# Kernel optimization log

Hardware: AMD Instinct MI355X
Metric: run time of the kernel (lower is better)

## Reference

```python
import jax, jax.numpy as jnp
import numpy as np

N, E, D, H = 15000, 300000, 128, 4
Dh = D // H
EPS = 1e-5

def gelu(x):
    return jax.nn.gelu(x, approximate=False)

def lin(x, W, b=None):
    y = x @ W.T
    return y + b if b is not None else y

def bnorm(x, g, b):
    # BatchNorm1d (training stats, biased var) over the row dim
    m = x.mean(0)
    v = x.var(0)
    return (x - m) * jax.lax.rsqrt(v + EPS) * g + b

def setup_inputs() -> dict:
    key = jax.random.key(0)
    ks = iter(jax.random.split(key, 64))
    def W(o, i):
        return jax.random.normal(next(ks), (o, i), jnp.float32) / jnp.sqrt(i)
    z = lambda o: jnp.zeros((o,), jnp.float32)
    o1 = lambda o: jnp.ones((o,), jnp.float32)
    inp = {
        'h_V': jax.random.normal(next(ks), (N, D), jnp.float32),
        'h_E': jax.random.normal(next(ks), (E, D), jnp.float32),
        'edge_idx': jax.random.randint(next(ks), (2, E), 0, N, jnp.int64),
        'batch_id': jnp.sort(jax.random.randint(next(ks), (N,), 0, 30, jnp.int32)),
        # NeighborAttention.W_V MLP: num_in(256)->128->128->128
        'Wv1': W(D, 2 * D), 'bv1': z(D), 'Wv2': W(D, D), 'bv2': z(D), 'Wv3': W(D, D), 'bv3': z(D),
        # NeighborAttention.Bias MLP: 3*128->128->128->num_heads
        'Wb1': W(D, 3 * D), 'bb1': z(D), 'Wb2': W(D, D), 'bb2': z(D), 'Wb3': W(H, D), 'bb3': z(H),
        # W_O (no bias)
        'Wo': W(D, D),
        # norms 0/1 on nodes
        'g0': o1(D), 'b0': z(D), 'g1': o1(D), 'b1': z(D),
        # dense FFN 128->512->128
        'Wd1': W(4 * D, D), 'bd1': z(4 * D), 'Wd2': W(D, 4 * D), 'bd2': z(D),
        # EdgeMLP: 384->128->128->128 plus edge norm
        'We1': W(D, 3 * D), 'be1': z(D), 'We2': W(D, D), 'be2': z(D), 'We3': W(D, D), 'be3': z(D),
        'ge': o1(D), 'bEn': z(D),
    }
    return inp

def reference(h_V, h_E, edge_idx, batch_id,
              Wv1, bv1, Wv2, bv2, Wv3, bv3,
              Wb1, bb1, Wb2, bb2, Wb3, bb3,
              Wo, g0, b0, g1, b1,
              Wd1, bd1, Wd2, bd2,
              We1, be1, We2, be2, We3, be3, ge, bEn):
    src, dst = edge_idx[0], edge_idx[1]
    # --- NeighborAttention (sparse) ---
    h_EV = jnp.concatenate([h_E, h_V[dst]], axis=-1)              # (E, 2D)
    bias_in = jnp.concatenate([h_V[src], h_EV], axis=-1)          # (E, 3D)
    w = lin(gelu(lin(gelu(lin(bias_in, Wb1, bb1)), Wb2, bb2)), Wb3, bb3)
    w = w * (1.0 / jnp.sqrt(jnp.float32(Dh)))                     # (E, H)
    V = lin(gelu(lin(gelu(lin(h_EV, Wv1, bv1)), Wv2, bv2)), Wv3, bv3).reshape(E, H, Dh)
    # scatter_softmax over edges grouped by src (center_id)
    m = jax.ops.segment_max(w, src, num_segments=N)               # (N, H)
    e = jnp.exp(w - m[src])
    s = jax.ops.segment_sum(e, src, num_segments=N)
    attend = e / s[src]                                           # (E, H)
    agg = jax.ops.segment_sum(attend[..., None] * V, src, num_segments=N).reshape(N, D)
    dh = agg @ Wo.T
    # --- residual + norm + FFN ---
    h_V = bnorm(h_V + dh, g0, b0)
    dh = lin(gelu(lin(h_V, Wd1, bd1)), Wd2, bd2)
    h_V = bnorm(h_V + dh, g1, b1)
    # --- EdgeMLP update ---
    h_EV2 = jnp.concatenate([h_V[src], h_E, h_V[dst]], axis=-1)   # (E, 3D)
    msg = lin(gelu(lin(gelu(lin(h_EV2, We1, be1)), We2, be2)), We3, be3)
    h_E = bnorm(h_E + msg, ge, bEn)
    # Context with node_context=edge_context=0 is a no-op
    return h_V, h_E
```

## Files before the change

### kernel.cpp

```cpp
#include <hip/hip_runtime.h>
#include <hip/hip_bf16.h>
#include <math.h>


#define NN 15000
#define EE 300000

typedef short s16x8 __attribute__((ext_vector_type(8)));
typedef float f32x4 __attribute__((ext_vector_type(4)));
#define MFMA16(a,b,c) __builtin_amdgcn_mfma_f32_16x16x32_bf16((a),(b),(c),0,0,0)

#define O_Wot  0
#define O_Wd1t (O_Wot  + 128*128)
#define O_Wd2t (O_Wd1t + 128*512)
#define O_BF   (O_Wd2t + 512*128)
#define O_WB   (O_BF + 107520)
#define O_M    (O_WB + EE*4)
#define O_S    (O_M + NN*4)
#define O_AGG  (O_S + NN*4)
#define O_STAT (O_AGG + NN*128)
#define O_AB   (O_STAT + 768)
#define O_XB   (O_AB + 768)
#define O_HID  (O_XB + NN*128)
#define O_PERM (O_HID + NN*512)
#define O_CNT  (O_PERM + EE)
#define O_CUR  (O_CNT + 15360)

#define UB_Wb1 0
#define UB_Wb2 49152
#define UB_Wb3 65536
#define UB_Wv1 67584
#define UB_Wv2 100352
#define UB_Wv3 116736
#define UB_We1 133120
#define UB_We2 182272
#define UB_We3 198656

__device__ inline float gelu_f(float x){
  return 0.5f*x*(1.0f + erff(x*0.70710678118654752f));
}
__device__ inline unsigned fenc(float f){
  unsigned u = __float_as_uint(f);
  return (u & 0x80000000u) ? ~u : (u | 0x80000000u);
}
__device__ inline float fdec(unsigned u){
  return __uint_as_float((u & 0x80000000u) ? (u & 0x7fffffffu) : ~u);
}
__device__ inline ushort bfb(float f){
  __bf16 h = (__bf16)f;
  return __builtin_bit_cast(unsigned short, h);
}


struct EMem {
  ushort act[128][128];
  int   idx[256];
  float cp[256];
};

struct EMemC {
  union { ushort act[128][128]; float vbuf[128][128]; };
  int pe[128];
  int idx[256];
};

union FB { s16x8 v; ushort u[8]; };

__device__ inline s16x8 load_x8(const float* __restrict__ p){
  float4 a = *(const float4*)p;
  float4 b = *(const float4*)(p+4);
  FB r;
  r.u[0]=bfb(a.x); r.u[1]=bfb(a.y); r.u[2]=bfb(a.z); r.u[3]=bfb(a.w);
  r.u[4]=bfb(b.x); r.u[5]=bfb(b.y); r.u[6]=bfb(b.z); r.u[7]=bfb(b.w);
  return r.v;
}

__device__ inline void st_act4(ushort (*act)[128], int e, int obase,
                               float g0,float g1,float g2,float g3){
  short4 s;
  s.x=(short)bfb(g0); s.y=(short)bfb(g1); s.z=(short)bfb(g2); s.w=(short)bfb(g3);
  *(short4*)&act[e][obase ^ ((e&7)<<3)] = s;
}
__device__ inline s16x8 ld_act(ushort (*act)[128], int e, int k0){
  return *(const s16x8*)&act[e][k0 ^ ((e&7)<<3)];
}

__device__ inline void zacc(f32x4 (&a)[4][4]){
  #pragma unroll
  for(int i=0;i<4;++i)
    #pragma unroll
    for(int j=0;j<4;++j) a[i][j] = (f32x4){0.f,0.f,0.f,0.f};
}

__device__ inline void mm_lds(const ushort* __restrict__ Wb, ushort (*act)[128],
                              int wm, int wn, int el, int kq, f32x4 (&acc)[4][4])
{
  #pragma unroll
  for (int kt=0; kt<4; ++kt){
    s16x8 af[4], bfr[4];
    #pragma unroll
    for (int mt=0;mt<4;++mt)
      af[mt] = *(const s16x8*)&Wb[(wm*64+mt*16+el)*128 + kt*32 + kq*8];
    #pragma unroll
    for (int nt=0;nt<4;++nt)
      bfr[nt] = ld_act(act, wn*64+nt*16+el, kt*32+kq*8);
    #pragma unroll
    for (int mt=0;mt<4;++mt)
      #pragma unroll
      for (int nt=0;nt<4;++nt)
        acc[mt][nt] = MFMA16(af[mt], bfr[nt], acc[mt][nt]);
  }
}

__device__ inline void intf(f32x4 (&acc)[4][4], const float* __restrict__ bias,
                            ushort (*act)[128], int wm, int wn, int el, int kq)
{
  #pragma unroll
  for (int mt=0;mt<4;++mt){
    int obase = wm*64+mt*16+kq*4;
    float4 bb = *(const float4*)&bias[obase];
    #pragma unroll
    for (int nt=0;nt<4;++nt){
      int e = wn*64+nt*16+el;
      st_act4(act, e, obase,
        gelu_f(acc[mt][nt][0]+bb.x), gelu_f(acc[mt][nt][1]+bb.y),
        gelu_f(acc[mt][nt][2]+bb.z), gelu_f(acc[mt][nt][3]+bb.w));
    }
  }
}

__device__ inline void edge_l1_3seg(const float* __restrict__ gV, const float* __restrict__ gI,
    const int* idx, const ushort* __restrict__ W1, int rowbase,
    int wm, int wn, int el, int kq, f32x4 (&acc)[4][4])
{
  #pragma unroll
  for (int seg=0; seg<3; ++seg){
    const float* rp[4];
    #pragma unroll
    for (int nt=0; nt<4; ++nt){
      int eloc = wn*64+nt*16+el;
      int g;
      if (seg==0) g = idx[eloc];
      else if (seg==1){ int e=rowbase+eloc; g = (e<EE)?e:(EE-1); }
      else g = idx[128+eloc];
      rp[nt] = ((seg==1)?gI:gV) + (size_t)g*128 + kq*8;
    }
    #pragma unroll
    for (int kt=0; kt<4; ++kt){
      s16x8 af[4], bfr[4];
      #pragma unroll
      for (int mt=0;mt<4;++mt)
        af[mt] = *(const s16x8*)&W1[(wm*64+mt*16+el)*384 + seg*128 + kt*32 + kq*8];
      #pragma unroll
      for (int nt=0;nt<4;++nt)
        bfr[nt] = load_x8(rp[nt] + kt*32);
      #pragma unroll
      for (int mt=0;mt<4;++mt)
        #pragma unroll
        for (int nt=0;nt<4;++nt)
          acc[mt][nt] = MFMA16(af[mt], bfr[nt], acc[mt][nt]);
    }
  }
}

__global__ void kHist(const int* __restrict__ eidx, int* __restrict__ cnt){
  int e = blockIdx.x*256 + threadIdx.x;
  if (e < EE) atomicAdd(&cnt[eidx[e]], 1);
}

__global__ void kScan(const int* __restrict__ cnt, int* __restrict__ cur){
  __shared__ int part[256];
  __shared__ int excl[256];
  int t = threadIdx.x;
  int base = t*60;
  int s = 0;
  for (int i=0;i<60;++i) s += cnt[base+i];
  part[t] = s;
  __syncthreads();
  if (t==0){ int r=0; for (int i=0;i<256;++i){ excl[i]=r; r+=part[i]; } }
  __syncthreads();
  int run = excl[t];
  for (int i=0;i<60;++i){ int c = cnt[base+i]; cur[base+i] = run; run += c; }
}

__global__ void kScat(const int* __restrict__ eidx, int* __restrict__ cur,
                      int* __restrict__ perm){
  int e = blockIdx.x*256 + threadIdx.x;
  if (e < EE){
    int p = atomicAdd(&cur[eidx[e]], 1);
    perm[p] = e;
  }
}

__global__ void kA_mfma(const float* __restrict__ hV, const float* __restrict__ hE,
    const int* __restrict__ eidx,
    const ushort* __restrict__ W1, const ushort* __restrict__ W2, const ushort* __restrict__ W3,
    const float* __restrict__ b1, const float* __restrict__ b2, const float* __restrict__ b3,
    float* __restrict__ wbuf, unsigned* __restrict__ mArr)
{
  __shared__ EMem sm;
  int t = threadIdx.x, lane = t&63, wave = t>>6;
  int el = lane&15, kq = lane>>4, wm = wave>>1, wn = wave&1;
  int rowbase = blockIdx.x*128;
  if (t<128){ int e=rowbase+t; if(e>=EE) e=EE-1; sm.idx[t]=eidx[e]; sm.idx[128+t]=eidx[EE+e]; }
  __syncthreads();
  f32x4 acc[4][4]; zacc(acc);
  edge_l1_3seg(hV, hE, sm.idx, W1, rowbase, wm, wn, el, kq, acc);
  intf(acc, b1, sm.act, wm, wn, el, kq);
  __syncthreads();
  zacc(acc);
  mm_lds(W2, sm.act, wm, wn, el, kq, acc);
  __syncthreads();
  intf(acc, b2, sm.act, wm, wn, el, kq);
  __syncthreads();
  f32x4 a3[2]; a3[0]=(f32x4){0.f,0.f,0.f,0.f}; a3[1]=(f32x4){0.f,0.f,0.f,0.f};
  #pragma unroll
  for (int kt=0;kt<4;++kt){
    s16x8 af = *(const s16x8*)&W3[el*128 + kt*32 + kq*8];
    #pragma unroll
    for (int q=0;q<2;++q){
      s16x8 bv = ld_act(sm.act, wave*32+q*16+el, kt*32+kq*8);
      a3[q] = MFMA16(af, bv, a3[q]);
    }
  }
  if (kq==0){
    #pragma unroll
    for (int q=0;q<2;++q){
      int eloc = wave*32+q*16+el, e = rowbase+eloc;
      if (e<EE){
        const float SC = 0.17677669529663687f;
        float4 w;
        w.x=(a3[q][0]+b3[0])*SC; w.y=(a3[q][1]+b3[1])*SC;
        w.z=(a3[q][2]+b3[2])*SC; w.w=(a3[q][3]+b3[3])*SC;
        *(float4*)&wbuf[e*4] = w;
        unsigned s4 = (unsigned)sm.idx[eloc]*4;
        atomicMax(&mArr[s4+0],fenc(w.x));
        atomicMax(&mArr[s4+1],fenc(w.y));
        atomicMax(&mArr[s4+2],fenc(w.z));
        atomicMax(&mArr[s4+3],fenc(w.w));
      }
    }
  }
}

__global__ void kB(const int* __restrict__ eidx, const unsigned* __restrict__ mArr,
                   float* __restrict__ wbuf, float* __restrict__ sArr)
{
  int tid = blockIdx.x*256 + threadIdx.x;
  if (tid >= EE*4) return;
  int e = tid >> 2, h = tid & 3;
  int srcn = eidx[e];
  float ex = expf(wbuf[tid] - fdec(mArr[srcn*4 + h]));
  wbuf[tid] = ex;
  atomicAdd(&sArr[srcn*4 + h], ex);
}

__global__ void kC_mfma(const float* __restrict__ hV, const float* __restrict__ hE,
    const int* __restrict__ eidx, const int* __restrict__ perm,
    const ushort* __restrict__ W1, const ushort* __restrict__ W2, const ushort* __restrict__ W3,
    const float* __restrict__ b1, const float* __restrict__ b2, const float* __restrict__ b3,
    const float* __restrict__ wbuf, const float* __restrict__ sArr,
    float* __restrict__ agg)
{
  __shared__ EMemC sm;
  int t = threadIdx.x, lane = t&63, wave = t>>6;
  int el = lane&15, kq = lane>>4, wm = wave>>1, wn = wave&1;
  int rowbase = blockIdx.x*128;
  if (t<128){
    int slot = rowbase + t; if (slot >= EE) slot = EE-1;
    int pe = perm[slot];
    sm.pe[t] = pe;
    sm.idx[t] = eidx[pe];
    sm.idx[128+t] = eidx[EE+pe];
  }
  __syncthreads();
  f32x4 acc[4][4]; zacc(acc);
  #pragma unroll
  for (int seg=0; seg<2; ++seg){
    const float* rp[4];
    #pragma unroll
    for (int nt=0; nt<4; ++nt){
      int eloc = wn*64+nt*16+el;
      int g = (seg==0) ? sm.pe[eloc] : sm.idx[128+eloc];
      rp[nt] = ((seg==0)?hE:hV) + (size_t)g*128 + kq*8;
    }
    #pragma unroll
    for (int kt=0; kt<4; ++kt){
      s16x8 af[4], bfr[4];
      #pragma unroll
      for (int mt=0;mt<4;++mt)
        af[mt] = *(const s16x8*)&W1[(wm*64+mt*16+el)*256 + seg*128 + kt*32 + kq*8];
      #pragma unroll
      for (int nt=0;nt<4;++nt)
        bfr[nt] = load_x8(rp[nt] + kt*32);
      #pragma unroll
      for (int mt=0;mt<4;++mt)
        #pragma unroll
        for (int nt=0;nt<4;++nt)
          acc[mt][nt] = MFMA16(af[mt], bfr[nt], acc[mt][nt]);
    }
  }
  intf(acc, b1, sm.act, wm, wn, el, kq);
  __syncthreads();
  zacc(acc);
  mm_lds(W2, sm.act, wm, wn, el, kq, acc);
  __syncthreads();
  intf(acc, b2, sm.act, wm, wn, el, kq);
  __syncthreads();
  zacc(acc);
  mm_lds(W3, sm.act, wm, wn, el, kq, acc);
  __syncthreads();
  #pragma unroll
  for (int nt=0;nt<4;++nt){
    int e = wn*64+nt*16+el;
    int slot = rowbase + e;
    float at4[4];
    if (slot < EE){
      int pe = sm.pe[e];
      int sn = sm.idx[e];
      float4 wv = *(const float4*)&wbuf[pe*4];
      float4 sv = *(const float4*)&sArr[sn*4];
      at4[0]=wv.x/sv.x; at4[1]=wv.y/sv.y; at4[2]=wv.z/sv.z; at4[3]=wv.w/sv.w;
    } else {
      at4[0]=at4[1]=at4[2]=at4[3]=0.f;
    }
    #pragma unroll
    for (int mt=0;mt<4;++mt){
      int o = wm*64+mt*16+kq*4;
      float4 bb = *(const float4*)&b3[o];
      float a = at4[o>>5];
      float4 v;
      v.x = a*(acc[mt][nt][0]+bb.x);
      v.y = a*(acc[mt][nt][1]+bb.y);
      v.z = a*(acc[mt][nt][2]+bb.z);
      v.w = a*(acc[mt][nt][3]+bb.w);
      *(float4*)&sm.vbuf[e][o ^ ((e&7)<<2)] = v;
    }
  }
  __syncthreads();
  {
    int col = t & 127, h2 = t >> 7;
    int e0 = h2*64;
    float run = 0.f;
    int cursrc = sm.idx[e0];
    for (int e = e0; e < e0+64; ++e){
      int s = sm.idx[e];
      if (s != cursrc){
        atomicAdd(&agg[(size_t)cursrc*128 + col], run);
        run = 0.f; cursrc = s;
      }
      run += sm.vbuf[e][col ^ ((e&7)<<2)];
    }
    atomicAdd(&agg[(size_t)cursrc*128 + col], run);
  }
}

__global__ void kI_mfma(const float* __restrict__ hVfin, const float* __restrict__ hE,
    const int* __restrict__ eidx,
    const ushort* __restrict__ W1, const ushort* __restrict__ W2, const ushort* __restrict__ W3,
    const float* __restrict__ b1, const float* __restrict__ b2, const float* __restrict__ b3,
    float* __restrict__ hEout, float* __restrict__ stat)
{
  __shared__ EMem sm;
  int t = threadIdx.x, lane = t&63, wave = t>>6;
  int el = lane&15, kq = lane>>4, wm = wave>>1, wn = wave&1;
  int rowbase = blockIdx.x*128;
  if (t<128){ int e=rowbase+t; if(e>=EE) e=EE-1; sm.idx[t]=eidx[e]; sm.idx[128+t]=eidx[EE+e]; }
  __syncthreads();
  f32x4 acc[4][4]; zacc(acc);
  edge_l1_3seg(hVfin, hE, sm.idx, W1, rowbase, wm, wn, el, kq, acc);
  intf(acc, b1, sm.act, wm, wn, el, kq);
  __syncthreads();
  zacc(acc);
  mm_lds(W2, sm.act, wm, wn, el, kq, acc);
  __syncthreads();
  intf(acc, b2, sm.act, wm, wn, el, kq);
  __syncthreads();
  zacc(acc);
  mm_lds(W3, sm.act, wm, wn, el, kq, acc);
  float ps[4][4], pq[4][4];
  #pragma unroll
  for (int mt=0;mt<4;++mt)
    #pragma unroll
    for (int r=0;r<4;++r){ ps[mt][r]=0.f; pq[mt][r]=0.f; }
  #pragma unroll
  for (int nt=0;nt<4;++nt){
    int eloc = wn*64+nt*16+el, e = rowbase+eloc;
    if (e < EE){
      #pragma unroll
      for (int mt=0;mt<4;++mt){
        int o = wm*64+mt*16+kq*4;
        float4 bb = *(const float4*)&b3[o];
        float4 h0 = *(const float4*)&hE[(size_t)e*128+o];
        float4 v;
        v.x = h0.x+acc[mt][nt][0]+bb.x;
        v.y = h0.y+acc[mt][nt][1]+bb.y;
        v.z = h0.z+acc[mt][nt][2]+bb.z;
        v.w = h0.w+acc[mt][nt][3]+bb.w;
        *(float4*)&hEout[(size_t)e*128+o] = v;
        ps[mt][0]+=v.x; ps[mt][1]+=v.y; ps[mt][2]+=v.z; ps[mt][3]+=v.w;
        pq[mt][0]+=v.x*v.x; pq[mt][1]+=v.y*v.y; pq[mt][2]+=v.z*v.z; pq[mt][3]+=v.w*v.w;
      }
    }
  }
  __syncthreads();
  sm.cp[t] = 0.f;
  __syncthreads();
  #pragma unroll
  for (int mt=0;mt<4;++mt){
    int o = wm*64+mt*16+kq*4;
    #pragma unroll
    for (int r=0;r<4;++r){
      atomicAdd(&sm.cp[o+r], ps[mt][r]);
      atomicAdd(&sm.cp[128+o+r], pq[mt][r]);
    }
  }
  __syncthreads();
  atomicAdd(&stat[t], sm.cp[t]);
}

struct SMem {
  float act[128][132];
  float ws[16][128];
  int   idx[256];
  float cp[256];
};

__device__ inline void zero8(float (&a)[8][8]){
  #pragma unroll
  for (int i=0;i<8;++i)
    #pragma unroll
    for (int j=0;j<8;++j) a[i][j]=0.f;
}

__device__ inline void stage_chunk(const float* __restrict__ src, int width, int kbase,
                                   const int* idxArr, int rowbase, int limit,
                                   float (*act)[132], int t)
{
  __syncthreads();
  int k = t & 127, half = t >> 7;
  const float* sp = src + kbase + k;
  #pragma unroll
  for (int i = 0; i < 64; i += 4){
    int r = half*64 + i;
    float v[4];
    #pragma unroll
    for (int j = 0; j < 4; ++j){
      int rr = r + j;
      int g = idxArr ? idxArr[rr] : ((rowbase + rr < limit) ? (rowbase + rr) : (limit-1));
      v[j] = sp[g*width];
    }
    *(float4*)&act[k][r] = make_float4(v[0],v[1],v[2],v[3]);
  }
  __syncthreads();
}

__device__ inline void stage_aff(const float* __restrict__ src, const float* __restrict__ ab,
                                 int rowbase, int limit, float (*act)[132], int t)
{
  __syncthreads();
  int k = t & 127, half = t >> 7;
  float a = ab[k], c = ab[128+k];
  const float* sp = src + k;
  #pragma unroll
  for (int i = 0; i < 64; i += 4){
    int r = half*64 + i;
    float v[4];
    #pragma unroll
    for (int j = 0; j < 4; ++j){
      int rr = r + j;
      int g = (rowbase + rr < limit) ? (rowbase + rr) : (limit-1);
      v[j] = fmaf(sp[g*128], a, c);
    }
    *(float4*)&act[k][r] = make_float4(v[0],v[1],v[2],v[3]);
  }
  __syncthreads();
}

__device__ inline void gemm128(const float* __restrict__ Wt, int ldw, int kbase, int ccol,
                               float (&acc)[8][8], float (*act)[132], float (*ws)[128], int t)
{
  int c0 = (t & 15)*8, r0 = (t >> 4)*8;
  for (int ks = 0; ks < 128; ks += 16){
    __syncthreads();
    {
      int kk = t >> 4, c = (t & 15)*8;
      const float* wp = Wt + (kbase + ks + kk)*ldw + ccol + c;
      float4 w0 = *(const float4*)wp;
      float4 w1 = *(const float4*)(wp + 4);
      *(float4*)&ws[kk][c]   = w0;
      *(float4*)&ws[kk][c+4] = w1;
    }
    __syncthreads();
    #pragma unroll
    for (int kk = 0; kk < 16; ++kk){
      int k = ks + kk;
      float4 xa = *(float4*)&act[k][r0];
      float4 xb = *(float4*)&act[k][r0+4];
      float4 wa = *(float4*)&ws[kk][c0];
      float4 wb = *(float4*)&ws[kk][c0+4];
      float x[8] = {xa.x,xa.y,xa.z,xa.w,xb.x,xb.y,xb.z,xb.w};
      float w[8] = {wa.x,wa.y,wa.z,wa.w,wb.x,wb.y,wb.z,wb.w};
      #pragma unroll
      for (int ri=0;ri<8;++ri)
        #pragma unroll
        for (int ci=0;ci<8;++ci)
          acc[ri][ci] = fmaf(x[ri], w[ci], acc[ri][ci]);
    }
  }
}

__device__ inline void block_stats(const float (&ps)[8], const float (&pq)[8],
                                   float* __restrict__ stat, float* cp, int t)
{
  int c0=(t&15)*8;
  __syncthreads();
  cp[t] = 0.f;
  __syncthreads();
  #pragma unroll
  for (int ci=0;ci<8;++ci){
    atomicAdd(&cp[c0+ci], ps[ci]);
    atomicAdd(&cp[128+c0+ci], pq[ci]);
  }
  __syncthreads();
  if (t < 128){
    atomicAdd(&stat[t], cp[t]);
    atomicAdd(&stat[128+t], cp[128+t]);
  }
}

struct TP { const float* s[3]; float* d[3]; };

__global__ void kT(TP a){
  const int Os[3]={128,512,128};
  const int Is[3]={128,128,512};
  int b = blockIdx.x, mi = 0, off = 0;
  for (;;){
    int nb = (Os[mi]*Is[mi] + 4095) >> 12;
    if (b < off + nb) break;
    off += nb; ++mi;
  }
  int O = Os[mi], I = Is[mi], sz = O*I;
  int e0 = (b - off) * 4096;
  int eEnd = (e0 + 4096 < sz) ? (e0 + 4096) : sz;
  for (int e = e0 + (int)threadIdx.x; e < eEnd; e += 256){
    int o = e / I, i = e - o*I;
    a.d[mi][i*O + o] = a.s[mi][e];
  }
}

struct CP9 { const float* s[9]; };

__global__ void kConv(CP9 a, ushort* __restrict__ dst){
  const int SZ[9]   = {49152,16384,2048,32768,16384,16384,49152,16384,16384};
  const int SRCSZ[9]= {49152,16384, 512,32768,16384,16384,49152,16384,16384};
  int b = blockIdx.x, mi=0, off=0;
  for(;;){ int nb=(SZ[mi]+1023)>>10; if (b<off+nb) break; off+=nb; ++mi; }
  int base=0;
  for(int j=0;j<mi;++j) base+=SZ[j];
  int e0=(b-off)*1024;
  int eE=(e0+1024<SZ[mi])?(e0+1024):SZ[mi];
  for (int i=e0+(int)threadIdx.x; i<eE; i+=256){
    float v = (i < SRCSZ[mi]) ? a.s[mi][i] : 0.f;
    dst[base+i] = bfb(v);
  }
}

__global__ __launch_bounds__(256,2) void kD(
    const float* __restrict__ hV, const float* __restrict__ aggM, const float* __restrict__ Wot,
    float* __restrict__ xbuf, float* __restrict__ stat)
{
  __shared__ SMem sm;
  int t = threadIdx.x;
  int rowbase = blockIdx.x * 128;
  float acc[8][8];
  zero8(acc);
  stage_chunk(aggM, 128, 0, nullptr, rowbase, NN, sm.act, t);
  gemm128(Wot, 128, 0, 0, acc, sm.act, sm.ws, t);
  int c0=(t&15)*8, r0=(t>>4)*8;
  float ps[8]={0,0,0,0,0,0,0,0}, pq[8]={0,0,0,0,0,0,0,0};
  #pragma unroll
  for (int ri=0;ri<8;++ri){
    int g = rowbase + r0 + ri;
    if (g < NN){
      float4 h0 = *(const float4*)&hV[g*128+c0];
      float4 h1 = *(const float4*)&hV[g*128+c0+4];
      float hv[8]={h0.x,h0.y,h0.z,h0.w,h1.x,h1.y,h1.z,h1.w};
      float v[8];
      #pragma unroll
      for (int ci=0;ci<8;++ci){
        v[ci]=hv[ci]+acc[ri][ci];
        ps[ci]+=v[ci]; pq[ci]+=v[ci]*v[ci];
      }
      *(float4*)&xbuf[g*128+c0]   = make_float4(v[0],v[1],v[2],v[3]);
      *(float4*)&xbuf[g*128+c0+4] = make_float4(v[4],v[5],v[6],v[7]);
    }
  }
  block_stats(ps,pq,stat,sm.cp,t);
}

__global__ void kFin(const float* __restrict__ stat, const float* __restrict__ gw,
                     const float* __restrict__ bw, float* __restrict__ ab, float invcnt)
{
  int t = threadIdx.x;
  float mean = stat[t]*invcnt;
  float var  = fmaxf(stat[128+t]*invcnt - mean*mean, 0.f);
  float inv  = rsqrtf(var + 1e-5f);
  float a = inv * gw[t];
  ab[t] = a;
  ab[128+t] = fmaf(-mean, a, bw[t]);
}

__global__ __launch_bounds__(256,2) void kF1(
    const float* __restrict__ xbuf, const float* __restrict__ ab0,
    const float* __restrict__ Wd1t, const float* __restrict__ bd1,
    float* __restrict__ hidden)
{
  __shared__ SMem sm;
  int t = threadIdx.x;
  int rowbase = blockIdx.x * 128;
  stage_aff(xbuf, ab0, rowbase, NN, sm.act, t);
  int c0=(t&15)*8, r0=(t>>4)*8;
  for (int cc=0; cc<4; ++cc){
    float acc[8][8];
    zero8(acc);
    gemm128(Wd1t, 512, 0, cc*128, acc, sm.act, sm.ws, t);
    float bd[8];
    #pragma unroll
    for (int ci=0;ci<8;++ci) bd[ci]=bd1[cc*128+c0+ci];
    #pragma unroll
    for (int ri=0;ri<8;++ri){
      int g = rowbase + r0 + ri;
      if (g < NN){
        float v[8];
        #pragma unroll
        for (int ci=0;ci<8;++ci) v[ci]=gelu_f(acc[ri][ci]+bd[ci]);
        *(float4*)&hidden[g*512+cc*128+c0]   = make_float4(v[0],v[1],v[2],v[3]);
        *(float4*)&hidden[g*512+cc*128+c0+4] = make_float4(v[4],v[5],v[6],v[7]);
      }
    }
  }
}

__global__ __launch_bounds__(256,2) void kF2(
    const float* __restrict__ xbuf, const float* __restrict__ hidden,
    const float* __restrict__ ab0, const float* __restrict__ Wd2t, const float* __restrict__ bd2,
    float* __restrict__ hVout, float* __restrict__ stat)
{
  __shared__ SMem sm;
  int t = threadIdx.x;
  int rowbase = blockIdx.x * 128;
  float acc[8][8];
  zero8(acc);
  for (int cc=0; cc<4; ++cc){
    stage_chunk(hidden, 512, cc*128, nullptr, rowbase, NN, sm.act, t);
    gemm128(Wd2t, 128, cc*128, 0, acc, sm.act, sm.ws, t);
  }
  int c0=(t&15)*8, r0=(t>>4)*8;
  float a0v[8],c0v[8],bd[8];
  #pragma unroll
  for (int ci=0;ci<8;++ci){ a0v[ci]=ab0[c0+ci]; c0v[ci]=ab0[128+c0+ci]; bd[ci]=bd2[c0+ci]; }
  float ps[8]={0,0,0,0,0,0,0,0}, pq[8]={0,0,0,0,0,0,0,0};
  #pragma unroll
  for (int ri=0;ri<8;++ri){
    int g = rowbase + r0 + ri;
    if (g < NN){
      float4 x0 = *(const float4*)&xbuf[g*128+c0];
      float4 x1 = *(const float4*)&xbuf[g*128+c0+4];
      float xv[8]={x0.x,x0.y,x0.z,x0.w,x1.x,x1.y,x1.z,x1.w};
      float v[8];
      #pragma unroll
      for (int ci=0;ci<8;++ci){
        v[ci] = fmaf(xv[ci], a0v[ci], c0v[ci]) + acc[ri][ci] + bd[ci];
        ps[ci]+=v[ci]; pq[ci]+=v[ci]*v[ci];
      }
      *(float4*)&hVout[g*128+c0]   = make_float4(v[0],v[1],v[2],v[3]);
      *(float4*)&hVout[g*128+c0+4] = make_float4(v[4],v[5],v[6],v[7]);
    }
  }
  block_stats(ps,pq,stat,sm.cp,t);
}

__global__ void kNorm(float* __restrict__ x, const float* __restrict__ ab, int total)
{
  int i = (blockIdx.x*256 + (int)threadIdx.x)*4;
  if (i >= total) return;
  float4 v = *(float4*)&x[i];
  int c = i & 127;
  v.x = fmaf(v.x, ab[c],   ab[128+c]);
  v.y = fmaf(v.y, ab[c+1], ab[128+c+1]);
  v.z = fmaf(v.z, ab[c+2], ab[128+c+2]);
  v.w = fmaf(v.w, ab[c+3], ab[128+c+3]);
  *(float4*)&x[i] = v;
}

extern "C" void kernel_launch(void* const* d_in, const int* in_sizes, int n_in,
                              void* d_out, int out_size, void* d_ws, size_t ws_size,
                              hipStream_t stream)
{
  const float* hV  =(const float*)d_in[0];
  const float* hE  =(const float*)d_in[1];
  const int*   eidx=(const int*)  d_in[2];
  const float* Wv1 =(const float*)d_in[4];
  const float* bv1 =(const float*)d_in[5];
  const float* Wv2 =(const float*)d_in[6];
  const float* bv2 =(const float*)d_in[7];
  const float* Wv3 =(const float*)d_in[8];
  const float* bv3 =(const float*)d_in[9];
  const float* Wb1 =(const float*)d_in[10];
  const float* bb1 =(const float*)d_in[11];
  const float* Wb2 =(const float*)d_in[12];
  const float* bb2 =(const float*)d_in[13];
  const float* Wb3 =(const float*)d_in[14];
  const float* bb3 =(const float*)d_in[15];
  const float* Wo  =(const float*)d_in[16];
  const float* g0  =(const float*)d_in[17];
  const float* b0  =(const float*)d_in[18];
  const float* g1  =(const float*)d_in[19];
  const float* b1  =(const float*)d_in[20];
  const float* Wd1 =(const float*)d_in[21];
  const float* bd1 =(const float*)d_in[22];
  const float* Wd2 =(const float*)d_in[23];
  const float* bd2 =(const float*)d_in[24];
  const float* We1 =(const float*)d_in[25];
  const float* be1 =(const float*)d_in[26];
  const float* We2 =(const float*)d_in[27];
  const float* be2 =(const float*)d_in[28];
  const float* We3 =(const float*)d_in[29];
  const float* be3 =(const float*)d_in[30];
  const float* ge  =(const float*)d_in[31];
  const float* bEn =(const float*)d_in[32];

  float* W  = (float*)d_ws;
  float* dO = (float*)d_out;
  ushort* WB = (ushort*)(W + O_BF);

  TP tp;
  tp.s[0]=Wo;  tp.d[0]=W+O_Wot;
  tp.s[1]=Wd1; tp.d[1]=W+O_Wd1t;
  tp.s[2]=Wd2; tp.d[2]=W+O_Wd2t;
  kT<<<36,256,0,stream>>>(tp);

  CP9 c9;
  c9.s[0]=Wb1; c9.s[1]=Wb2; c9.s[2]=Wb3;
  c9.s[3]=Wv1; c9.s[4]=Wv2; c9.s[5]=Wv3;
  c9.s[6]=We1; c9.s[7]=We2; c9.s[8]=We3;
  kConv<<<210,256,0,stream>>>(c9, WB);

  hipMemsetAsync(W + O_CNT, 0, 15360*sizeof(int), stream);
  kHist<<<(EE+255)/256,256,0,stream>>>(eidx, (int*)(W+O_CNT));
  kScan<<<1,256,0,stream>>>((const int*)(W+O_CNT), (int*)(W+O_CUR));
  kScat<<<(EE+255)/256,256,0,stream>>>(eidx, (int*)(W+O_CUR), (int*)(W+O_PERM));

  hipMemsetAsync(W + O_M, 0, (size_t)(O_AB - O_M)*sizeof(float), stream);

  kA_mfma<<<(EE+127)/128,256,0,stream>>>(hV,hE,eidx, WB+UB_Wb1,WB+UB_Wb2,WB+UB_Wb3,
                                         bb1,bb2,bb3, W+O_WB,(unsigned*)(W+O_M));
  kB<<<(EE*4+255)/256,256,0,stream>>>(eidx,(const unsigned*)(W+O_M), W+O_WB, W+O_S);
  kC_mfma<<<(EE+127)/128,256,0,stream>>>(hV,hE,eidx,(const int*)(W+O_PERM),
                                         WB+UB_Wv1,WB+UB_Wv2,WB+UB_Wv3,
                                         bv1,bv2,bv3, W+O_WB, W+O_S, W+O_AGG);

  kD<<<(NN+127)/128,256,0,stream>>>(hV, W+O_AGG, W+O_Wot, W+O_XB, W+O_STAT);
  kFin<<<1,128,0,stream>>>(W+O_STAT, g0, b0, W+O_AB, 1.0f/NN);
  kF1<<<(NN+127)/128,256,0,stream>>>(W+O_XB, W+O_AB, W+O_Wd1t, bd1, W+O_HID);
  kF2<<<(NN+127)/128,256,0,stream>>>(W+O_XB, W+O_HID, W+O_AB, W+O_Wd2t, bd2,
                                     dO, W+O_STAT+256);
  kFin<<<1,128,0,stream>>>(W+O_STAT+256, g1, b1, W+O_AB+256, 1.0f/NN);
  kNorm<<<(NN*128/4+255)/256,256,0,stream>>>(dO, W+O_AB+256, NN*128);

  kI_mfma<<<(EE+127)/128,256,0,stream>>>(dO, hE, eidx, WB+UB_We1,WB+UB_We2,WB+UB_We3,
                                         be1,be2,be3, dO+(size_t)NN*128, W+O_STAT+512);
  kFin<<<1,128,0,stream>>>(W+O_STAT+512, ge, bEn, W+O_AB+512, 1.0f/EE);
  kNorm<<<(EE*128/4+255)/256,256,0,stream>>>(dO+(size_t)NN*128, W+O_AB+512, EE*128);
}
```

Baseline: 1.642 ms.

## Split edge MLP tiles across 8 waves with 512-thread blocks

The three edge-MLP MFMA kernels now run 512-thread blocks of 8 waves instead of 4 over the same 128-edge tile. Each wave computes a 64x32 output sub-tile, which halves the accumulator registers per wave. Launch bounds are added to encourage more waves in flight and better latency hiding for the gathered global loads. In exchange, each weight fragment is now loaded by twice as many waves, the final reductions are resized for the new wave layout, and the segmented scatter in kC produces more atomics.

```diff
diff --git a/kernel.cpp b/kernel.cpp
--- a/kernel.cpp
+++ b/kernel.cpp
@@ -85,34 +85,34 @@
   return *(const s16x8*)&act[e][k0 ^ ((e&7)<<3)];
 }
 
-__device__ inline void zacc(f32x4 (&a)[4][4]){
+__device__ inline void zacc(f32x4 (&a)[4][2]){
   #pragma unroll
   for(int i=0;i<4;++i)
     #pragma unroll
-    for(int j=0;j<4;++j) a[i][j] = (f32x4){0.f,0.f,0.f,0.f};
+    for(int j=0;j<2;++j) a[i][j] = (f32x4){0.f,0.f,0.f,0.f};
 }
 
 __device__ inline void mm_lds(const ushort* __restrict__ Wb, ushort (*act)[128],
-                              int wm, int wn, int el, int kq, f32x4 (&acc)[4][4])
+                              int wm, int wn, int el, int kq, f32x4 (&acc)[4][2])
 {
   #pragma unroll
   for (int kt=0; kt<4; ++kt){
-    s16x8 af[4], bfr[4];
+    s16x8 af[4], bfr[2];
     #pragma unroll
     for (int mt=0;mt<4;++mt)
       af[mt] = *(const s16x8*)&Wb[(wm*64+mt*16+el)*128 + kt*32 + kq*8];
     #pragma unroll
-    for (int nt=0;nt<4;++nt)
-      bfr[nt] = ld_act(act, wn*64+nt*16+el, kt*32+kq*8);
+    for (int nt=0;nt<2;++nt)
+      bfr[nt] = ld_act(act, wn*32+nt*16+el, kt*32+kq*8);
     #pragma unroll
     for (int mt=0;mt<4;++mt)
       #pragma unroll
-      for (int nt=0;nt<4;++nt)
+      for (int nt=0;nt<2;++nt)
         acc[mt][nt] = MFMA16(af[mt], bfr[nt], acc[mt][nt]);
   }
 }
 
-__device__ inline void intf(f32x4 (&acc)[4][4], const float* __restrict__ bias,
+__device__ inline void intf(f32x4 (&acc)[4][2], const float* __restrict__ bias,
                             ushort (*act)[128], int wm, int wn, int el, int kq)
 {
   #pragma unroll
@@ -120,8 +120,8 @@
     int obase = wm*64+mt*16+kq*4;
     float4 bb = *(const float4*)&bias[obase];
     #pragma unroll
-    for (int nt=0;nt<4;++nt){
-      int e = wn*64+nt*16+el;
+    for (int nt=0;nt<2;++nt){
+      int e = wn*32+nt*16+el;
       st_act4(act, e, obase,
         gelu_f(acc[mt][nt][0]+bb.x), gelu_f(acc[mt][nt][1]+bb.y),
         gelu_f(acc[mt][nt][2]+bb.z), gelu_f(acc[mt][nt][3]+bb.w));
@@ -131,14 +131,14 @@
 
 __device__ inline void edge_l1_3seg(const float* __restrict__ gV, const float* __restrict__ gI,
     const int* idx, const ushort* __restrict__ W1, int rowbase,
-    int wm, int wn, int el, int kq, f32x4 (&acc)[4][4])
+    int wm, int wn, int el, int kq, f32x4 (&acc)[4][2])
 {
   #pragma unroll
   for (int seg=0; seg<3; ++seg){
-    const float* rp[4];
-    #pragma unroll
-    for (int nt=0; nt<4; ++nt){
-      int eloc = wn*64+nt*16+el;
+    const float* rp[2];
+    #pragma unroll
+    for (int nt=0; nt<2; ++nt){
+      int eloc = wn*32+nt*16+el;
       int g;
       if (seg==0) g = idx[eloc];
       else if (seg==1){ int e=rowbase+eloc; g = (e<EE)?e:(EE-1); }
@@ -147,17 +147,17 @@
     }
     #pragma unroll
     for (int kt=0; kt<4; ++kt){
-      s16x8 af[4], bfr[4];
+      s16x8 af[4], bfr[2];
       #pragma unroll
       for (int mt=0;mt<4;++mt)
         af[mt] = *(const s16x8*)&W1[(wm*64+mt*16+el)*384 + seg*128 + kt*32 + kq*8];
       #pragma unroll
-      for (int nt=0;nt<4;++nt)
+      for (int nt=0;nt<2;++nt)
         bfr[nt] = load_x8(rp[nt] + kt*32);
       #pragma unroll
       for (int mt=0;mt<4;++mt)
         #pragma unroll
-        for (int nt=0;nt<4;++nt)
+        for (int nt=0;nt<2;++nt)
           acc[mt][nt] = MFMA16(af[mt], bfr[nt], acc[mt][nt]);
     }
   }
@@ -192,7 +192,8 @@
   }
 }
 
-__global__ void kA_mfma(const float* __restrict__ hV, const float* __restrict__ hE,
+__global__ __launch_bounds__(512,4) void kA_mfma(
+    const float* __restrict__ hV, const float* __restrict__ hE,
     const int* __restrict__ eidx,
     const ushort* __restrict__ W1, const ushort* __restrict__ W2, const ushort* __restrict__ W3,
     const float* __restrict__ b1, const float* __restrict__ b2, const float* __restrict__ b3,
@@ -200,11 +201,11 @@
 {
   __shared__ EMem sm;
   int t = threadIdx.x, lane = t&63, wave = t>>6;
-  int el = lane&15, kq = lane>>4, wm = wave>>1, wn = wave&1;
+  int el = lane&15, kq = lane>>4, wm = wave>>2, wn = wave&3;
   int rowbase = blockIdx.x*128;
   if (t<128){ int e=rowbase+t; if(e>=EE) e=EE-1; sm.idx[t]=eidx[e]; sm.idx[128+t]=eidx[EE+e]; }
   __syncthreads();
-  f32x4 acc[4][4]; zacc(acc);
+  f32x4 acc[4][2]; zacc(acc);
   edge_l1_3seg(hV, hE, sm.idx, W1, rowbase, wm, wn, el, kq, acc);
   intf(acc, b1, sm.act, wm, wn, el, kq);
   __syncthreads();
@@ -213,32 +214,26 @@
   __syncthreads();
   intf(acc, b2, sm.act, wm, wn, el, kq);
   __syncthreads();
-  f32x4 a3[2]; a3[0]=(f32x4){0.f,0.f,0.f,0.f}; a3[1]=(f32x4){0.f,0.f,0.f,0.f};
+  f32x4 a3 = (f32x4){0.f,0.f,0.f,0.f};
   #pragma unroll
   for (int kt=0;kt<4;++kt){
     s16x8 af = *(const s16x8*)&W3[el*128 + kt*32 + kq*8];
-    #pragma unroll
-    for (int q=0;q<2;++q){
-      s16x8 bv = ld_act(sm.act, wave*32+q*16+el, kt*32+kq*8);
-      a3[q] = MFMA16(af, bv, a3[q]);
-    }
+    s16x8 bv = ld_act(sm.act, wave*16+el, kt*32+kq*8);
+    a3 = MFMA16(af, bv, a3);
   }
   if (kq==0){
-    #pragma unroll
-    for (int q=0;q<2;++q){
-      int eloc = wave*32+q*16+el, e = rowbase+eloc;
-      if (e<EE){
-        const float SC = 0.17677669529663687f;
-        float4 w;
-        w.x=(a3[q][0]+b3[0])*SC; w.y=(a3[q][1]+b3[1])*SC;
-        w.z=(a3[q][2]+b3[2])*SC; w.w=(a3[q][3]+b3[3])*SC;
-        *(float4*)&wbuf[e*4] = w;
-        unsigned s4 = (unsigned)sm.idx[eloc]*4;
-        atomicMax(&mArr[s4+0],fenc(w.x));
-        atomicMax(&mArr[s4+1],fenc(w.y));
-        atomicMax(&mArr[s4+2],fenc(w.z));
-        atomicMax(&mArr[s4+3],fenc(w.w));
-      }
+    int eloc = wave*16+el, e = rowbase+eloc;
+    if (e<EE){
+      const float SC = 0.17677669529663687f;
+      float4 w;
+      w.x=(a3[0]+b3[0])*SC; w.y=(a3[1]+b3[1])*SC;
+      w.z=(a3[2]+b3[2])*SC; w.w=(a3[3]+b3[3])*SC;
+      *(float4*)&wbuf[e*4] = w;
+      unsigned s4 = (unsigned)sm.idx[eloc]*4;
+      atomicMax(&mArr[s4+0],fenc(w.x));
+      atomicMax(&mArr[s4+1],fenc(w.y));
+      atomicMax(&mArr[s4+2],fenc(w.z));
+      atomicMax(&mArr[s4+3],fenc(w.w));
     }
   }
 }
@@ -255,7 +250,8 @@
   atomicAdd(&sArr[srcn*4 + h], ex);
 }
 
-__global__ void kC_mfma(const float* __restrict__ hV, const float* __restrict__ hE,
+__global__ __launch_bounds__(512,4) void kC_mfma(
+    const float* __restrict__ hV, const float* __restrict__ hE,
     const int* __restrict__ eidx, const int* __restrict__ perm,
     const ushort* __restrict__ W1, const ushort* __restrict__ W2, const ushort* __restrict__ W3,
     const float* __restrict__ b1, const float* __restrict__ b2, const float* __restrict__ b3,
@@ -264,7 +260,7 @@
 {
   __shared__ EMemC sm;
   int t = threadIdx.x, lane = t&63, wave = t>>6;
-  int el = lane&15, kq = lane>>4, wm = wave>>1, wn = wave&1;
+  int el = lane&15, kq = lane>>4, wm = wave>>2, wn = wave&3;
   int rowbase = blockIdx.x*128;
   if (t<128){
     int slot = rowbase + t; if (slot >= EE) slot = EE-1;
@@ -274,29 +270,29 @@
     sm.idx[128+t] = eidx[EE+pe];
   }
   __syncthreads();
-  f32x4 acc[4][4]; zacc(acc);
+  f32x4 acc[4][2]; zacc(acc);
   #pragma unroll
   for (int seg=0; seg<2; ++seg){
-    const float* rp[4];
-    #pragma unroll
-    for (int nt=0; nt<4; ++nt){
-      int eloc = wn*64+nt*16+el;
+    const float* rp[2];
+    #pragma unroll
+    for (int nt=0; nt<2; ++nt){
+      int eloc = wn*32+nt*16+el;
       int g = (seg==0) ? sm.pe[eloc] : sm.idx[128+eloc];
       rp[nt] = ((seg==0)?hE:hV) + (size_t)g*128 + kq*8;
     }
     #pragma unroll
     for (int kt=0; kt<4; ++kt){
-      s16x8 af[4], bfr[4];
+      s16x8 af[4], bfr[2];
       #pragma unroll
       for (int mt=0;mt<4;++mt)
         af[mt] = *(const s16x8*)&W1[(wm*64+mt*16+el)*256 + seg*128 + kt*32 + kq*8];
       #pragma unroll
-      for (int nt=0;nt<4;++nt)
+      for (int nt=0;nt<2;++nt)
         bfr[nt] = load_x8(rp[nt] + kt*32);
       #pragma unroll
       for (int mt=0;mt<4;++mt)
         #pragma unroll
-        for (int nt=0;nt<4;++nt)
+        for (int nt=0;nt<2;++nt)
           acc[mt][nt] = MFMA16(af[mt], bfr[nt], acc[mt][nt]);
     }
   }
@@ -311,8 +307,8 @@
   mm_lds(W3, sm.act, wm, wn, el, kq, acc);
   __syncthreads();
   #pragma unroll
-  for (int nt=0;nt<4;++nt){
-    int e = wn*64+nt*16+el;
+  for (int nt=0;nt<2;++nt){
+    int e = wn*32+nt*16+el;
     int slot = rowbase + e;
     float at4[4];
     if (slot < EE){
@@ -339,11 +335,11 @@
   }
   __syncthreads();
   {
-    int col = t & 127, h2 = t >> 7;
-    int e0 = h2*64;
+    int col = t & 127, q2 = t >> 7;
+    int e0 = q2*32;
     float run = 0.f;
     int cursrc = sm.idx[e0];
-    for (int e = e0; e < e0+64; ++e){
+    for (int e = e0; e < e0+32; ++e){
       int s = sm.idx[e];
       if (s != cursrc){
         atomicAdd(&agg[(size_t)cursrc*128 + col], run);
@@ -355,7 +351,8 @@
   }
 }
 
-__global__ void kI_mfma(const float* __restrict__ hVfin, const float* __restrict__ hE,
+__global__ __launch_bounds__(512,4) void kI_mfma(
+    const float* __restrict__ hVfin, const float* __restrict__ hE,
     const int* __restrict__ eidx,
     const ushort* __restrict__ W1, const ushort* __restrict__ W2, const ushort* __restrict__ W3,
     const float* __restrict__ b1, const float* __restrict__ b2, const float* __restrict__ b3,
@@ -363,11 +360,11 @@
 {
   __shared__ EMem sm;
   int t = threadIdx.x, lane = t&63, wave = t>>6;
-  int el = lane&15, kq = lane>>4, wm = wave>>1, wn = wave&1;
+  int el = lane&15, kq = lane>>4, wm = wave>>2, wn = wave&3;
   int rowbase = blockIdx.x*128;
   if (t<128){ int e=rowbase+t; if(e>=EE) e=EE-1; sm.idx[t]=eidx[e]; sm.idx[128+t]=eidx[EE+e]; }
   __syncthreads();
-  f32x4 acc[4][4]; zacc(acc);
+  f32x4 acc[4][2]; zacc(acc);
   edge_l1_3seg(hVfin, hE, sm.idx, W1, rowbase, wm, wn, el, kq, acc);
   intf(acc, b1, sm.act, wm, wn, el, kq);
   __syncthreads();
@@ -384,8 +381,8 @@
     #pragma unroll
     for (int r=0;r<4;++r){ ps[mt][r]=0.f; pq[mt][r]=0.f; }
   #pragma unroll
-  for (int nt=0;nt<4;++nt){
-    int eloc = wn*64+nt*16+el, e = rowbase+eloc;
+  for (int nt=0;nt<2;++nt){
+    int eloc = wn*32+nt*16+el, e = rowbase+eloc;
     if (e < EE){
       #pragma unroll
       for (int mt=0;mt<4;++mt){
@@ -404,7 +401,7 @@
     }
   }
   __syncthreads();
-  sm.cp[t] = 0.f;
+  if (t < 256) sm.cp[t] = 0.f;
   __syncthreads();
   #pragma unroll
   for (int mt=0;mt<4;++mt){
@@ -416,7 +413,7 @@
     }
   }
   __syncthreads();
-  atomicAdd(&stat[t], sm.cp[t]);
+  if (t < 256) atomicAdd(&stat[t], sm.cp[t]);
 }
 
 struct SMem {
@@ -754,10 +751,10 @@
 
   hipMemsetAsync(W + O_M, 0, (size_t)(O_AB - O_M)*sizeof(float), stream);
 
-  kA_mfma<<<(EE+127)/128,256,0,stream>>>(hV,hE,eidx, WB+UB_Wb1,WB+UB_Wb2,WB+UB_Wb3,
+  kA_mfma<<<(EE+127)/128,512,0,stream>>>(hV,hE,eidx, WB+UB_Wb1,WB+UB_Wb2,WB+UB_Wb3,
                                          bb1,bb2,bb3, W+O_WB,(unsigned*)(W+O_M));
   kB<<<(EE*4+255)/256,256,0,stream>>>(eidx,(const unsigned*)(W+O_M), W+O_WB, W+O_S);
-  kC_mfma<<<(EE+127)/128,256,0,stream>>>(hV,hE,eidx,(const int*)(W+O_PERM),
+  kC_mfma<<<(EE+127)/128,512,0,stream>>>(hV,hE,eidx,(const int*)(W+O_PERM),
                                          WB+UB_Wv1,WB+UB_Wv2,WB+UB_Wv3,
                                          bv1,bv2,bv3, W+O_WB, W+O_S, W+O_AGG);
 
@@ -769,7 +766,7 @@
   kFin<<<1,128,0,stream>>>(W+O_STAT+256, g1, b1, W+O_AB+256, 1.0f/NN);
   kNorm<<<(NN*128/4+255)/256,256,0,stream>>>(dO, W+O_AB+256, NN*128);
 
-  kI_mfma<<<(EE+127)/128,256,0,stream>>>(dO, hE, eidx, WB+UB_We1,WB+UB_We2,WB+UB_We3,
+  kI_mfma<<<(EE+127)/128,512,0,stream>>>(dO, hE, eidx, WB+UB_We1,WB+UB_We2,WB+UB_We3,
                                          be1,be2,be3, dO+(size_t)NN*128, W+O_STAT+512);
   kFin<<<1,128,0,stream>>>(W+O_STAT+512, ge, bEn, W+O_AB+512, 1.0f/EE);
   kNorm<<<(EE*128/4+255)/256,256,0,stream>>>(dO+(size_t)NN*128, W+O_AB+512, EE*128);
```

After: 1.840 ms. 1.12x slower.
